# Performance work log

Measured on AMD Instinct MI355X. Metric: run time of the kernel, lower is better.

Reference implementation:

```python
import jax, jax.numpy as jnp
import numpy as np

B, S, DIM, NQ, NKV = 2, 2048, 4096, 32, 8
HD = DIM // NQ  # 128


def _rope(t, fc):
    # t: [B,S,H,D]; fc: [S,D/2,2] = (cos,sin). Complex multiply on (even,odd) pairs.
    b, s, h, d = t.shape
    tp = t.astype(jnp.float32).reshape(b, s, h, d // 2, 2)
    c = fc[None, :, None, :, 0]
    sn = fc[None, :, None, :, 1]
    x0, x1 = tp[..., 0], tp[..., 1]
    rot = jnp.stack([x0 * c - x1 * sn, x0 * sn + x1 * c], axis=-1)
    return rot.reshape(b, s, h, d).astype(t.dtype)


def setup_inputs() -> dict:
    key = jax.random.key(0)
    ks = jax.random.split(key, 5)
    x = jax.random.normal(ks[0], (B, S, DIM), jnp.float32)
    wq = jax.random.normal(ks[1], (DIM, NQ * HD), jnp.float32) * 0.02
    wk = jax.random.normal(ks[2], (DIM, NKV * HD), jnp.float32) * 0.02
    wv = jax.random.normal(ks[3], (DIM, NKV * HD), jnp.float32) * 0.02
    wo = jax.random.normal(ks[4], (NQ * HD, DIM), jnp.float32) * 0.02
    # Llama RoPE frequencies for positions [0, S)
    inv_freq = 1.0 / (10000.0 ** (jnp.arange(0, HD, 2, dtype=jnp.float32) / HD))
    ang = jnp.arange(S, dtype=jnp.float32)[:, None] * inv_freq[None, :]  # [S, HD/2]
    freqs_cis = jnp.stack([jnp.cos(ang), jnp.sin(ang)], axis=-1)  # [S, HD/2, 2]
    cache_key = jnp.zeros((B, S, NKV, HD), jnp.float32)
    cache_value = jnp.zeros((B, S, NKV, HD), jnp.float32)
    return {"x": x, "start_pos": 0, "freqs_cis": freqs_cis, "wq": wq, "wk": wk,
            "wv": wv, "wo": wo, "cache_key": cache_key, "cache_value": cache_value}


def reference(x, start_pos, freqs_cis, wq, wk, wv, wo, cache_key, cache_value):
    b, s, dim = x.shape
    nkv, hd = cache_key.shape[2], cache_key.shape[3]
    nq = wq.shape[1] // hd
    n_rep = nq // nkv
    xq = (x @ wq).reshape(b, s, nq, hd)
    xk = (x @ wk).reshape(b, s, nkv, hd)
    xv = (x @ wv).reshape(b, s, nkv, hd)
    xq = _rope(xq, freqs_cis)
    xk = _rope(xk, freqs_cis)
    # KV-cache write then read of the valid prefix
    ck = jax.lax.dynamic_update_slice(cache_key, xk, (0, start_pos, 0, 0))
    cv = jax.lax.dynamic_update_slice(cache_value, xv, (0, start_pos, 0, 0))
    kv_len = start_pos + s
    k = ck[:, :kv_len]
    v = cv[:, :kv_len]
    # GQA: repeat_interleave kv heads to match q heads (as original materializes)
    keys = jnp.repeat(k, n_rep, axis=2)    # [B,K,NQ,HD]
    values = jnp.repeat(v, n_rep, axis=2)
    scale = 1.0 / jnp.sqrt(jnp.float32(hd))
    scores = jnp.einsum('bqhd,bkhd->bhqk', xq, keys) * scale  # [B,H,S,K]
    attn = jax.nn.softmax(scores, axis=-1)  # NOTE: no causal mask, as in source
    out = jnp.einsum('bhqk,bkhd->bqhd', attn, values).reshape(b, s, nq * hd)
    return out @ wo
```

## Files before the change

kernel.cpp:

```cpp
#include <hip/hip_runtime.h>
#include <stdint.h>


typedef __attribute__((ext_vector_type(8))) short short8;
typedef __attribute__((ext_vector_type(4))) float f32x4;
typedef __attribute__((ext_vector_type(16))) float f32x16;

#define DEVFN static __device__ __forceinline__

DEVFN ushort f2bf(float f) {
  uint32_t u = __builtin_bit_cast(uint32_t, f);
  u += 0x7fffu + ((u >> 16) & 1);
  return (ushort)(u >> 16);
}

DEVFN uint32_t pkbf(float a, float b) {
  return (uint32_t)f2bf(a) | ((uint32_t)f2bf(b) << 16);
}

DEVFN void gll16(const void* g, void* l) {
  __builtin_amdgcn_global_load_lds(
      (const __attribute__((address_space(1))) void*)g,
      (__attribute__((address_space(3))) void*)l, 16, 0, 0);
}

DEVFN float xhalf_max(float v) { return fmaxf(v, __shfl_xor(v, 32)); }
DEVFN float xhalf_add(float v) { return v + __shfl_xor(v, 32); }

DEVFN short8 mk_frag(uint32_t w0, uint32_t w1, uint32_t w2, uint32_t w3, int hi) {
  uint32_t x0 = __shfl_xor(w0, 32);
  uint32_t x1 = __shfl_xor(w1, 32);
  uint32_t x2 = __shfl_xor(w2, 32);
  uint32_t x3 = __shfl_xor(w3, 32);
  uint4 u;
  u.x = hi ? x2 : w0;
  u.y = hi ? x3 : w1;
  u.z = hi ? w2 : x0;
  u.w = hi ? w3 : x1;
  return __builtin_bit_cast(short8, u);
}

__global__ __launch_bounds__(256) void k_cvt(const float* __restrict__ src,
                                             ushort* __restrict__ dst, int n8) {
  int i = blockIdx.x * 256 + threadIdx.x;
  if (i >= n8) return;
  const float4* s4 = (const float4*)src + (size_t)i * 2;
  float4 a = s4[0], b = s4[1];
  uint4 o;
  o.x = (uint32_t)f2bf(a.x) | ((uint32_t)f2bf(a.y) << 16);
  o.y = (uint32_t)f2bf(a.z) | ((uint32_t)f2bf(a.w) << 16);
  o.z = (uint32_t)f2bf(b.x) | ((uint32_t)f2bf(b.y) << 16);
  o.w = (uint32_t)f2bf(b.z) | ((uint32_t)f2bf(b.w) << 16);
  ((uint4*)dst)[i] = o;
}

__global__ __launch_bounds__(256) void k_tr(const float* __restrict__ src,
                                            ushort* __restrict__ dst, int R, int C) {
  __shared__ float tile[64][65];
  const int c0 = blockIdx.x * 64, r0 = blockIdx.y * 64;
  const int t = threadIdx.x, rr = t >> 6, cc = t & 63;
#pragma unroll
  for (int i = 0; i < 16; ++i)
    tile[rr + i * 4][cc] = src[(size_t)(r0 + rr + i * 4) * C + c0 + cc];
  __syncthreads();
#pragma unroll
  for (int i = 0; i < 16; ++i)
    dst[(size_t)(c0 + rr + i * 4) * R + r0 + cc] = f2bf(tile[cc][rr + i * 4]);
}

template <int MODE>
__global__ __launch_bounds__(512, 2) void k_gemm8(
    const ushort* __restrict__ A, const ushort* __restrict__ Bp,
    const float* __restrict__ fcis, ushort* __restrict__ oQ,
    ushort* __restrict__ oK, ushort* __restrict__ oV, float* __restrict__ oC) {
  constexpr int K = 4096;
  constexpr int BN = MODE ? 256 : 192;
  constexpr int WN = BN / 4;
  constexpr int NF = WN / 16;
  constexpr int NBX = MODE ? 16 : 32;
  constexpr int ABUF = 16384;
  constexpr int BBUF = BN * 64;
  constexpr int NT = K / 32;

  __shared__ char smem[4 * ABUF + 4 * BBUF];
  char* AsL = smem;
  char* BsL = smem + 4 * ABUF;

  constexpr int nwg = NBX * 16;
  const int bid = blockIdx.x;
  const int wg = (bid & 7) * (nwg >> 3) + (bid >> 3);
  const int nb = wg % NBX, mb = wg / NBX;
  const int m0 = mb * 256, n0 = nb * BN;

  const int tid = threadIdx.x;
  const int w = tid >> 6, lane = tid & 63;
  const int gg = lane >> 4, rr = lane & 15;
  const int wm = w >> 2, wn = w & 3;

  const int l8 = lane >> 3, s7 = lane & 7;
  const int Ra0 = w * 8 + l8, Ra1 = 64 + Ra0;
  const int ea0 = s7 ^ (Ra0 & 7), ea1 = s7 ^ (Ra1 & 7);
  const ushort* agp0 = A + (size_t)(m0 + 2 * Ra0 + (ea0 >> 2)) * K + (ea0 & 3) * 8;
  const ushort* agp1 = A + (size_t)(m0 + 2 * Ra1 + (ea1 >> 2)) * K + (ea1 & 3) * 8;
  char* lda0 = AsL + w * 1024;
  char* lda1 = AsL + 8192 + w * 1024;

  const int Rb0 = w * 8 + l8;
  const int eb0 = s7 ^ (Rb0 & 7);
  const ushort* bgp0 = Bp + (size_t)(n0 + 2 * Rb0 + (eb0 >> 2)) * K + (eb0 & 3) * 8;
  char* ldb0 = BsL + w * 1024;
  const int Rb1 = MODE ? (64 + w * 8 + l8) : (64 + w * 4 + l8);
  const int eb1 = s7 ^ (Rb1 & 7);
  const ushort* bgp1 = Bp + (size_t)(n0 + 2 * Rb1 + (eb1 >> 2)) * K + (eb1 & 3) * 8;
  char* ldb1 = BsL + 8192 + (MODE ? w * 1024 : w * 512);

  auto STAGE = [&](int t) {
    const int bo = t & 3;
    const size_t ko = (size_t)t * 32;
    gll16(agp0 + ko, lda0 + bo * ABUF);
    gll16(agp1 + ko, lda1 + bo * ABUF);
    gll16(bgp0 + ko, ldb0 + bo * BBUF);
    if constexpr (MODE) {
      gll16(bgp1 + ko, ldb1 + bo * BBUF);
    } else {
      if (lane < 32) gll16(bgp1 + ko, ldb1 + bo * BBUF);
    }
  };

  int aoff[8], boff[NF];
#pragma unroll
  for (int mf = 0; mf < 8; ++mf) {
    const int m = wm * 128 + mf * 16 + rr;
    aoff[mf] = (m >> 1) * 128 + (((((m & 1) << 2) | gg) ^ ((m >> 1) & 7)) << 4);
  }
#pragma unroll
  for (int nf = 0; nf < NF; ++nf) {
    const int n = wn * WN + nf * 16 + rr;
    boff[nf] = (n >> 1) * 128 + (((((n & 1) << 2) | gg) ^ ((n >> 1) & 7)) << 4);
  }

  f32x4 acc[8][NF] = {};

  auto COMPUTE = [&](int bo) {
    const char* Ab = AsL + bo * ABUF;
    const char* Bb = BsL + bo * BBUF;
    short8 bfr[NF];
#pragma unroll
    for (int nf = 0; nf < NF; ++nf) bfr[nf] = *(const short8*)(Bb + boff[nf]);
#pragma unroll
    for (int mf = 0; mf < 8; ++mf) {
      short8 a = *(const short8*)(Ab + aoff[mf]);
#pragma unroll
      for (int nf = 0; nf < NF; ++nf)
        acc[mf][nf] =
            __builtin_amdgcn_mfma_f32_16x16x32_bf16(a, bfr[nf], acc[mf][nf], 0, 0, 0);
    }
  };

  STAGE(0);
  STAGE(1);
  STAGE(2);
  asm volatile("s_waitcnt vmcnt(8)" ::: "memory");
  __builtin_amdgcn_s_barrier();
  __builtin_amdgcn_sched_barrier(0);

  for (int t = 0; t < NT - 3; ++t) {
    STAGE(t + 3);
    __builtin_amdgcn_s_setprio(1);
    COMPUTE(t & 3);
    __builtin_amdgcn_s_setprio(0);
    asm volatile("s_waitcnt vmcnt(8)" ::: "memory");
    __builtin_amdgcn_s_barrier();
    __builtin_amdgcn_sched_barrier(0);
  }
  __builtin_amdgcn_s_setprio(1);
  COMPUTE((NT - 3) & 3);
  __builtin_amdgcn_s_setprio(0);
  asm volatile("s_waitcnt vmcnt(4)" ::: "memory");
  __builtin_amdgcn_s_barrier();
  __builtin_amdgcn_sched_barrier(0);
  __builtin_amdgcn_s_setprio(1);
  COMPUTE((NT - 2) & 3);
  __builtin_amdgcn_s_setprio(0);
  asm volatile("s_waitcnt vmcnt(0)" ::: "memory");
  __builtin_amdgcn_s_barrier();
  __builtin_amdgcn_sched_barrier(0);
  __builtin_amdgcn_s_setprio(1);
  COMPUTE((NT - 1) & 3);
  __builtin_amdgcn_s_setprio(0);

  if constexpr (MODE == 1) {
#pragma unroll
    for (int mf = 0; mf < 8; ++mf) {
      const int mbase = m0 + wm * 128 + mf * 16 + gg * 4;
#pragma unroll
      for (int nf = 0; nf < NF; ++nf) {
        const int n = n0 + wn * WN + nf * 16 + rr;
#pragma unroll
        for (int j = 0; j < 4; ++j)
          oC[(size_t)(mbase + j) * 4096 + n] = acc[mf][nf][j];
      }
    }
  } else {
    const int b = m0 >> 11;
#pragma unroll
    for (int mf = 0; mf < 8; ++mf) {
      const int mbase = m0 + wm * 128 + mf * 16 + gg * 4;
      const int s0 = mbase & 2047;
#pragma unroll
      for (int nf = 0; nf < NF; ++nf) {
        const int n = n0 + wn * WN + nf * 16 + rr;
        if (n < 5120) {
          const int d = n & 127, ii = d >> 1;
          const float sgn = (n & 1) ? 1.0f : -1.0f;
          const float qsc = (n < 4096) ? 0.12752364599362f : 1.0f;
          ushort res[4];
#pragma unroll
          for (int j = 0; j < 4; ++j) {
            const float2 cs = ((const float2*)fcis)[(size_t)(s0 + j) * 64 + ii];
            float v = acc[mf][nf][j];
            float pv = __shfl_xor(v, 1);
            res[j] = f2bf(qsc * (v * cs.x + sgn * pv * cs.y));
          }
          if (n < 4096) {
            ushort* dst = oQ + ((size_t)(b * 32 + (n >> 7)) * 2048 + s0) * 128 + d;
#pragma unroll
            for (int j = 0; j < 4; ++j) dst[j * 128] = res[j];
          } else {
            ushort* dst =
                oK + ((size_t)(b * 8 + ((n - 4096) >> 7)) * 2048 + s0) * 128 + d;
#pragma unroll
            for (int j = 0; j < 4; ++j) dst[j * 128] = res[j];
          }
        } else {
          const int n2 = n - 5120;
          ushort4 pk;
          pk.x = f2bf(acc[mf][nf][0]);
          pk.y = f2bf(acc[mf][nf][1]);
          pk.z = f2bf(acc[mf][nf][2]);
          pk.w = f2bf(acc[mf][nf][3]);
          *(ushort4*)&oV[((size_t)(b * 8 + (n2 >> 7)) * 128 + (n2 & 127)) * 2048 + s0] =
              pk;
        }
      }
    }
  }
}

__global__ __launch_bounds__(512, 2) void k_attn(const ushort* __restrict__ Qg,
                                                 const ushort* __restrict__ Kg,
                                                 const ushort* __restrict__ Vt,
                                                 ushort* __restrict__ Og) {
  __shared__ ushort Ks[2][64 * 128];
  __shared__ ushort Vs[2][64 * 128];
  __shared__ float sml[8][32];

  const int bh = blockIdx.x, qt = blockIdx.y;
  const int b = bh >> 5, h = bh & 31, hk = h >> 2;
  const int t = threadIdx.x, w = t >> 6, lane = t & 63;
  const int ln31 = lane & 31, hi = lane >> 5;
  const int q0 = qt * 256;

  short8 qf[8];
  {
    const size_t qbase = ((size_t)bh * 2048 + q0 + w * 32 + ln31) * 128;
#pragma unroll
    for (int tt = 0; tt < 8; ++tt)
      qf[tt] = *(const short8*)&Qg[qbase + tt * 16 + hi * 8];
  }
  const size_t kgb = (size_t)(b * 8 + hk) * 2048 * 128;
  const size_t vgb = (size_t)(b * 8 + hk) * 128 * 2048;

  const int srow = t >> 3;
  const int ssl = (t & 7) * 2;
  const int s0 = ssl ^ (srow & 15);
  const int vd = 2 * (t >> 3) + ((t & 7) >> 2);
  const int vkl = (t & 3) * 16;
  const ushort* kgp = Kg + kgb + (size_t)srow * 128 + ssl * 8;
  const ushort* vgp = Vt + vgb + (size_t)vd * 2048 + vkl;

  uint4 rk0, rk1, rv0, rv1;
  auto LOAD = [&](int k0) {
    const uint4* kp = (const uint4*)(kgp + (size_t)k0 * 128);
    rk0 = kp[0];
    rk1 = kp[1];
    const uint4* vp = (const uint4*)(vgp + k0);
    rv0 = vp[0];
    rv1 = vp[1];
  };
  auto STORE = [&](int buf) {
    char* kd = (char*)Ks[buf] + srow * 256;
    *(uint4*)(kd + (s0 << 4)) = rk0;
    *(uint4*)(kd + ((s0 ^ 1) << 4)) = rk1;
    char* vdd = (char*)Vs[buf] + srow * 256;
    *(uint4*)(vdd + (s0 << 4)) = rv0;
    *(uint4*)(vdd + ((s0 ^ 1) << 4)) = rv1;
  };

  f32x16 ov[4] = {};
  float m_run = -1e30f, l_run = 0.f;

  const int mk = ln31 & 15;
  const int krb0 = ln31 * 256, krb1 = krb0 + 8192;
  const int vrb = (ln31 >> 1) * 256;
  const int vsp = (ln31 & 1) * 8 + hi;
  const int mv = ln31 >> 1;

  LOAD(0);
  STORE(0);
  __syncthreads();

  for (int tile = 0; tile < 32; ++tile) {
    const int cur = tile & 1;
    if (tile < 31) LOAD((tile + 1) * 64);

    const char* Kc = (const char*)Ks[cur];
    f32x16 p0 = {}, p1 = {};
#pragma unroll
    for (int tt = 0; tt < 8; ++tt) {
      const int sl = ((tt * 2 + hi) ^ mk) << 4;
      short8 ka0 = *(const short8*)(Kc + krb0 + sl);
      short8 ka1 = *(const short8*)(Kc + krb1 + sl);
      p0 = __builtin_amdgcn_mfma_f32_32x32x16_bf16(ka0, qf[tt], p0, 0, 0, 0);
      p1 = __builtin_amdgcn_mfma_f32_32x32x16_bf16(ka1, qf[tt], p1, 0, 0, 0);
    }

    float vmx = p0[0];
#pragma unroll
    for (int i = 1; i < 16; ++i) vmx = fmaxf(vmx, p0[i]);
#pragma unroll
    for (int i = 0; i < 16; ++i) vmx = fmaxf(vmx, p1[i]);
    const float pmax = xhalf_max(vmx);
    if (!__all(pmax <= m_run + 8.0f)) {
      const float mnew = fmaxf(m_run, pmax);
      const float al = exp2f(m_run - mnew);
      m_run = mnew;
      l_run *= al;
      sml[w][ln31] = al;
      const float4 a0 = *(const float4*)&sml[w][hi * 4];
      const float4 a1 = *(const float4*)&sml[w][8 + hi * 4];
      const float4 a2 = *(const float4*)&sml[w][16 + hi * 4];
      const float4 a3 = *(const float4*)&sml[w][24 + hi * 4];
      const float aa[16] = {a0.x, a0.y, a0.z, a0.w, a1.x, a1.y, a1.z, a1.w,
                            a2.x, a2.y, a2.z, a2.w, a3.x, a3.y, a3.z, a3.w};
#pragma unroll
      for (int i = 0; i < 16; ++i) {
        ov[0][i] *= aa[i]; ov[1][i] *= aa[i];
        ov[2][i] *= aa[i]; ov[3][i] *= aa[i];
      }
    }
#pragma unroll
    for (int i = 0; i < 16; ++i) p0[i] = exp2f(p0[i] - m_run);
#pragma unroll
    for (int i = 0; i < 16; ++i) p1[i] = exp2f(p1[i] - m_run);
    float ls = 0.f;
#pragma unroll
    for (int i = 0; i < 16; ++i) ls += p0[i] + p1[i];
    l_run += xhalf_add(ls);

    short8 pa[4];
    pa[0] = mk_frag(pkbf(p0[0], p0[1]), pkbf(p0[2], p0[3]),
                    pkbf(p0[4], p0[5]), pkbf(p0[6], p0[7]), hi);
    pa[1] = mk_frag(pkbf(p0[8], p0[9]), pkbf(p0[10], p0[11]),
                    pkbf(p0[12], p0[13]), pkbf(p0[14], p0[15]), hi);
    pa[2] = mk_frag(pkbf(p1[0], p1[1]), pkbf(p1[2], p1[3]),
                    pkbf(p1[4], p1[5]), pkbf(p1[6], p1[7]), hi);
    pa[3] = mk_frag(pkbf(p1[8], p1[9]), pkbf(p1[10], p1[11]),
                    pkbf(p1[12], p1[13]), pkbf(p1[14], p1[15]), hi);

    const char* Vc = (const char*)Vs[cur];
#pragma unroll
    for (int db = 0; db < 4; ++db) {
      const int rb = vrb + db * 4096;
#pragma unroll
      for (int ks = 0; ks < 4; ++ks) {
        const int sl = ((vsp + ks * 2) ^ mv) << 4;
        short8 bv = *(const short8*)(Vc + rb + sl);
        ov[db] = __builtin_amdgcn_mfma_f32_32x32x16_bf16(pa[ks], bv, ov[db], 0, 0, 0);
      }
    }

    if (tile < 31) STORE(cur ^ 1);
    __syncthreads();
  }

  sml[w][ln31] = l_run;
  const float4 l0 = *(const float4*)&sml[w][hi * 4];
  const float4 l1 = *(const float4*)&sml[w][8 + hi * 4];
  const float4 l2 = *(const float4*)&sml[w][16 + hi * 4];
  const float4 l3 = *(const float4*)&sml[w][24 + hi * 4];
  const float inv[16] = {1.f / l0.x, 1.f / l0.y, 1.f / l0.z, 1.f / l0.w,
                         1.f / l1.x, 1.f / l1.y, 1.f / l1.z, 1.f / l1.w,
                         1.f / l2.x, 1.f / l2.y, 1.f / l2.z, 1.f / l2.w,
                         1.f / l3.x, 1.f / l3.y, 1.f / l3.z, 1.f / l3.w};
  const int qb0 = q0 + w * 32 + hi * 4;
#pragma unroll
  for (int rg = 0; rg < 4; ++rg)
#pragma unroll
    for (int j = 0; j < 4; ++j) {
      const int sq = qb0 + rg * 8 + j;
      const size_t orow = ((size_t)(b * 2048 + sq)) * 4096 + h * 128 + ln31;
#pragma unroll
      for (int db = 0; db < 4; ++db)
        Og[orow + db * 32] = f2bf(ov[db][rg * 4 + j] * inv[rg * 4 + j]);
    }
}

extern "C" void kernel_launch(void* const* d_in, const int* in_sizes, int n_in,
                              void* d_out, int out_size, void* d_ws, size_t ws_size,
                              hipStream_t stream) {
  const float* x = (const float*)d_in[0];
  const float* fcis = (const float*)d_in[2];
  const float* wq = (const float*)d_in[3];
  const float* wk = (const float*)d_in[4];
  const float* wv = (const float*)d_in[5];
  const float* wo = (const float*)d_in[6];
  float* out = (float*)d_out;

  char* ws = (char*)d_ws;
  ushort* xb  = (ushort*)(ws);
  ushort* wsT = (ushort*)(ws + 33554432u);
  ushort* qb  = (ushort*)(ws + 83886080u);
  ushort* kb  = (ushort*)(ws + 117440512u);
  ushort* vbT = (ushort*)(ws + 125829120u);
  ushort* woT = xb;
  ushort* ao  = wsT;

  k_cvt<<<8192, 256, 0, stream>>>(x, xb, 2097152);
  k_tr<<<dim3(64, 64), 256, 0, stream>>>(wq, wsT, 4096, 4096);
  k_tr<<<dim3(16, 64), 256, 0, stream>>>(wk, wsT + (size_t)4096 * 4096, 4096, 1024);
  k_tr<<<dim3(16, 64), 256, 0, stream>>>(wv, wsT + (size_t)5120 * 4096, 4096, 1024);
  k_gemm8<0><<<512, 512, 0, stream>>>(xb, wsT, fcis, qb, kb, vbT, nullptr);
  k_tr<<<dim3(64, 64), 256, 0, stream>>>(wo, woT, 4096, 4096);
  k_attn<<<dim3(64, 8), 512, 0, stream>>>(qb, kb, vbT, ao);
  k_gemm8<1><<<256, 512, 0, stream>>>(ao, woT, nullptr, nullptr, nullptr, nullptr,
                                      out);
}
```

Measured before the change: 588.3 us.

## Split GEMM K-step into two half-tiles interleaving A/B staging with MFMA

Each K-step of the bf16 GEMM main loop is split into two phases. Each phase loads half of the A fragments from LDS, issues part of the next tile's global-to-LDS loads (A then B), hits a barrier, and runs MFMAs at raised priority. This follows the ping-pong schedule used on CDNA, spreading memory issue across the compute and keeping fewer A fragments live in registers. The cost is extra workgroup barriers per K-step, which can add stalls.

```diff
diff --git a/kernel.cpp b/kernel.cpp
--- a/kernel.cpp
+++ b/kernel.cpp
@@ -39,6 +39,13 @@
   u.w = hi ? w3 : x1;
   return __builtin_bit_cast(short8, u);
 }
+
+#define VMW(N) asm volatile("s_waitcnt vmcnt(" #N ")" ::: "memory")
+#define SBAR()                        \
+  do {                                \
+    __builtin_amdgcn_s_barrier();     \
+    __builtin_amdgcn_sched_barrier(0);\
+  } while (0)
 
 __global__ __launch_bounds__(256) void k_cvt(const float* __restrict__ src,
                                              ushort* __restrict__ dst, int n8) {
@@ -114,11 +121,15 @@
   const ushort* bgp1 = Bp + (size_t)(n0 + 2 * Rb1 + (eb1 >> 2)) * K + (eb1 & 3) * 8;
   char* ldb1 = BsL + 8192 + (MODE ? w * 1024 : w * 512);
 
-  auto STAGE = [&](int t) {
+  auto STAGE_A = [&](int t) {
     const int bo = t & 3;
     const size_t ko = (size_t)t * 32;
     gll16(agp0 + ko, lda0 + bo * ABUF);
     gll16(agp1 + ko, lda1 + bo * ABUF);
+  };
+  auto STAGE_B = [&](int t) {
+    const int bo = t & 3;
+    const size_t ko = (size_t)t * 32;
     gll16(bgp0 + ko, ldb0 + bo * BBUF);
     if constexpr (MODE) {
       gll16(bgp1 + ko, ldb1 + bo * BBUF);
@@ -141,53 +152,58 @@
 
   f32x4 acc[8][NF] = {};
 
-  auto COMPUTE = [&](int bo) {
+  auto TILE = [&](int t, bool stg) {
+    const int bo = t & 3;
     const char* Ab = AsL + bo * ABUF;
     const char* Bb = BsL + bo * BBUF;
-    short8 bfr[NF];
+    short8 bfr[NF], afr[4];
 #pragma unroll
     for (int nf = 0; nf < NF; ++nf) bfr[nf] = *(const short8*)(Bb + boff[nf]);
 #pragma unroll
-    for (int mf = 0; mf < 8; ++mf) {
-      short8 a = *(const short8*)(Ab + aoff[mf]);
+    for (int i = 0; i < 4; ++i) afr[i] = *(const short8*)(Ab + aoff[i]);
+    if (stg) STAGE_A(t + 3);
+    SBAR();
+    __builtin_amdgcn_s_setprio(1);
+#pragma unroll
+    for (int mi = 0; mi < 4; ++mi)
 #pragma unroll
       for (int nf = 0; nf < NF; ++nf)
-        acc[mf][nf] =
-            __builtin_amdgcn_mfma_f32_16x16x32_bf16(a, bfr[nf], acc[mf][nf], 0, 0, 0);
-    }
+        acc[mi][nf] =
+            __builtin_amdgcn_mfma_f32_16x16x32_bf16(afr[mi], bfr[nf], acc[mi][nf], 0, 0, 0);
+    __builtin_amdgcn_s_setprio(0);
+    SBAR();
+#pragma unroll
+    for (int i = 0; i < 4; ++i) afr[i] = *(const short8*)(Ab + aoff[4 + i]);
+    if (stg) STAGE_B(t + 3);
+    SBAR();
+    __builtin_amdgcn_s_setprio(1);
+#pragma unroll
+    for (int mi = 0; mi < 4; ++mi)
+#pragma unroll
+      for (int nf = 0; nf < NF; ++nf)
+        acc[4 + mi][nf] =
+            __builtin_amdgcn_mfma_f32_16x16x32_bf16(afr[mi], bfr[nf], acc[4 + mi][nf], 0, 0, 0);
+    __builtin_amdgcn_s_setprio(0);
   };
 
-  STAGE(0);
-  STAGE(1);
-  STAGE(2);
-  asm volatile("s_waitcnt vmcnt(8)" ::: "memory");
-  __builtin_amdgcn_s_barrier();
-  __builtin_amdgcn_sched_barrier(0);
+  STAGE_A(0); STAGE_B(0);
+  STAGE_A(1); STAGE_B(1);
+  STAGE_A(2); STAGE_B(2);
+  VMW(8);
+  SBAR();
 
   for (int t = 0; t < NT - 3; ++t) {
-    STAGE(t + 3);
-    __builtin_amdgcn_s_setprio(1);
-    COMPUTE(t & 3);
-    __builtin_amdgcn_s_setprio(0);
-    asm volatile("s_waitcnt vmcnt(8)" ::: "memory");
-    __builtin_amdgcn_s_barrier();
-    __builtin_amdgcn_sched_barrier(0);
-  }
-  __builtin_amdgcn_s_setprio(1);
-  COMPUTE((NT - 3) & 3);
-  __builtin_amdgcn_s_setprio(0);
-  asm volatile("s_waitcnt vmcnt(4)" ::: "memory");
-  __builtin_amdgcn_s_barrier();
-  __builtin_amdgcn_sched_barrier(0);
-  __builtin_amdgcn_s_setprio(1);
-  COMPUTE((NT - 2) & 3);
-  __builtin_amdgcn_s_setprio(0);
-  asm volatile("s_waitcnt vmcnt(0)" ::: "memory");
-  __builtin_amdgcn_s_barrier();
-  __builtin_amdgcn_sched_barrier(0);
-  __builtin_amdgcn_s_setprio(1);
-  COMPUTE((NT - 1) & 3);
-  __builtin_amdgcn_s_setprio(0);
+    TILE(t, true);
+    VMW(8);
+    SBAR();
+  }
+  TILE(NT - 3, false);
+  VMW(4);
+  SBAR();
+  TILE(NT - 2, false);
+  VMW(0);
+  SBAR();
+  TILE(NT - 1, false);
 
   if constexpr (MODE == 1) {
 #pragma unroll
```

After: 588.4 us. Within noise of the previous version (+0.0%).
